# Optimization experiments

Hardware: AMD Instinct MI355X
Metric: run time of the kernel (lower is better)

Reference implementation:

```python
import jax, jax.numpy as jnp
import numpy as np


def setup_inputs() -> dict:
    key = jax.random.key(0)
    k1, k2 = jax.random.split(key)
    B, N, M = 8, 4096, 4096
    points1 = jax.random.normal(k1, (B, N, 3), dtype=jnp.float32)
    points2 = jax.random.normal(k2, (B, M, 3), dtype=jnp.float32)
    return {"points1": points1, "points2": points2}


def reference(points1, points2):
    x2 = jnp.sum(points1 * points1, axis=-1)            # [B, N]
    y2 = jnp.sum(points2 * points2, axis=-1)            # [B, M]
    xy = jnp.einsum('bnd,bmd->bnm', points1, points2)   # [B, N, M]
    d = x2[:, :, None] + y2[:, None, :] - 2.0 * xy      # [B, N, M]
    dist1 = jnp.min(d, axis=2)                          # [B, N] NN dist p1->p2
    dist2 = jnp.min(d, axis=1)                          # [B, M] NN dist p2->p1
    # Symmetric Hausdorff: max over each direction, then max of the two, sum over batch
    m = jnp.maximum(jnp.max(dist1, axis=-1), jnp.max(dist2, axis=-1))  # [B]
    return jnp.sum(m)
```

## Files before the change

### kernel.cpp

```cpp
#include <hip/hip_runtime.h>
#include <float.h>

#define B_CONST 8
#define ONE_BF 0x3F80

typedef short short8 __attribute__((ext_vector_type(8)));
typedef float f32x4  __attribute__((ext_vector_type(4)));

__device__ __forceinline__ unsigned short f2bf(float f) {
    unsigned u = __float_as_uint(f);
    return (unsigned short)((u + 0x7FFFu + ((u >> 16) & 1u)) >> 16);
}
__device__ __forceinline__ float bf2f(unsigned short h) {
    return __uint_as_float(((unsigned)h) << 16);
}
__device__ __forceinline__ float min3(float a, float b, float c) {
    float d;
    asm("v_min3_f32 %0, %1, %2, %3" : "=v"(d) : "v"(a), "v"(b), "v"(c));
    return d;
}

__global__ __launch_bounds__(256) void hd_mfma(
    const float* __restrict__ p1, const float* __restrict__ p2,
    float* __restrict__ part_row, float* __restrict__ part_col,
    unsigned int* __restrict__ comm, int N, int M) {
    int t = threadIdx.x;
    int blk = blockIdx.x;
    if (blk == 0 && t < 9) comm[t] = 0u;

    int gCount  = M >> 10;
    int rbCount = N >> 7;
    int perB = rbCount * gCount;
    int b   = blk / perB;
    int rem = blk - b * perB;
    int rb  = rem / gCount;
    int g   = rem - rb * gCount;

    __shared__ unsigned short ldsBlo[8192];
    __shared__ unsigned short ldsBhi[8192];
    __shared__ unsigned short ldsA0[1024];
    __shared__ unsigned short ldsA1[512];
    __shared__ unsigned int   ldsColU[1024];
    __shared__ float          ldsRow[128];
    __shared__ unsigned short ldsZero[8];

    if (t < 8) ldsZero[t] = 0;
    for (int i = t; i < 1024; i += 256) ldsColU[i] = 0x7F7FFFFFu;

    const float* rsrc = p2 + 3 * ((size_t)b * M + ((size_t)g << 10));
    for (int i = t; i < 1024; i += 256) {
        float x = rsrc[3*i], y = rsrc[3*i+1], z = rsrc[3*i+2];
        unsigned short hx = f2bf(x), hy = f2bf(y), hz = f2bf(z);
        float ex = x - bf2f(hx), ey = y - bf2f(hy), ez = z - bf2f(hz);
        unsigned short m2ex = f2bf(-2.f*ex), m2ey = f2bf(-2.f*ey), m2ez = f2bf(-2.f*ez);
        float rw = fmaf(x,x,fmaf(y,y,z*z));
        unsigned short hrw = f2bf(rw);
        unsigned short erw = f2bf(rw - bf2f(hrw));
        unsigned* lo = (unsigned*)(ldsBlo + i*8);
        lo[0] = hx | ((unsigned)hy << 16);
        lo[1] = hz | ((unsigned)hx << 16);
        lo[2] = hy | ((unsigned)hz << 16);
        lo[3] = m2ex | ((unsigned)m2ey << 16);
        unsigned* hi = (unsigned*)(ldsBhi + i*8);
        hi[0] = m2ez | ((unsigned)hrw << 16);
        hi[1] = erw | ((unsigned)ONE_BF << 16);
        hi[2] = ONE_BF;
        hi[3] = 0;
    }
    const float* qsrc = p1 + 3 * ((size_t)b * N + ((size_t)rb << 7));
    if (t < 128) {
        float x = qsrc[3*t], y = qsrc[3*t+1], z = qsrc[3*t+2];
        unsigned short hx = f2bf(x), hy = f2bf(y), hz = f2bf(z);
        float ex = x - bf2f(hx), ey = y - bf2f(hy), ez = z - bf2f(hz);
        float qw = fmaf(x,x,fmaf(y,y,z*z));
        unsigned short hqw = f2bf(qw);
        unsigned short eqw = f2bf(qw - bf2f(hqw));
        unsigned* a0 = (unsigned*)(ldsA0 + t*8);
        a0[0] = f2bf(-2.f*bf2f(hx)) | ((unsigned)f2bf(-2.f*bf2f(hy)) << 16);
        a0[1] = f2bf(-2.f*bf2f(hz)) | ((unsigned)f2bf(-2.f*ex) << 16);
        a0[2] = f2bf(-2.f*ey) | ((unsigned)f2bf(-2.f*ez) << 16);
        a0[3] = hx | ((unsigned)hy << 16);
        unsigned* a1 = (unsigned*)(ldsA1 + t*4);
        a1[0] = hz | ((unsigned)hqw << 16);
        a1[1] = eqw;
    }
    __syncthreads();

    int l = t & 63, w = t >> 6;
    int n = l & 15, quad = l >> 4;
    const unsigned short* bbase = (quad == 0) ? (ldsBlo + n*8)
                                : (quad == 1) ? (ldsBhi + n*8) : ldsZero;
    int bstride = (quad < 2) ? 128 : 0;

    f32x4 zacc = {0.f, 0.f, 0.f, 0.f};

    for (int s = w; s < 8; s += 4) {
        int qhat = (s << 4) + n;
        short8 af;
        {
            short8 a0v = *(const short8*)(ldsA0 + qhat*8);
            unsigned short hz_ = ldsA1[qhat*4], hqw = ldsA1[qhat*4+1], eqw = ldsA1[qhat*4+2];
            short8 ahi = { (short)hz_, (short)ONE_BF, (short)ONE_BF,
                           (short)hqw, (short)eqw, 0, 0, 0 };
            short8 az = {0,0,0,0,0,0,0,0};
            af = (quad == 0) ? a0v : (quad == 1) ? ahi : az;
        }
        float rm0 = FLT_MAX, rm1 = FLT_MAX, rm2 = FLT_MAX, rm3 = FLT_MAX;
        #pragma unroll 4
        for (int j = 0; j < 64; ++j) {
            short8 bf = *(const short8*)(bbase + j * bstride);
            f32x4 D = __builtin_amdgcn_mfma_f32_16x16x32_bf16(af, bf, zacc, 0, 0, 0);
            rm0 = fminf(rm0, D[0]); rm1 = fminf(rm1, D[1]);
            rm2 = fminf(rm2, D[2]); rm3 = fminf(rm3, D[3]);
            float cm = fminf(min3(D[0], D[1], D[2]), D[3]);
            atomicMin(&ldsColU[(j << 4) + n], __float_as_uint(cm));
        }
        #pragma unroll
        for (int msk = 1; msk < 16; msk <<= 1) {
            rm0 = fminf(rm0, __shfl_xor(rm0, msk, 64));
            rm1 = fminf(rm1, __shfl_xor(rm1, msk, 64));
            rm2 = fminf(rm2, __shfl_xor(rm2, msk, 64));
            rm3 = fminf(rm3, __shfl_xor(rm3, msk, 64));
        }
        if (n == 0) {
            float* rr = ldsRow + (s << 4) + (quad << 2);
            rr[0] = rm0; rr[1] = rm1; rr[2] = rm2; rr[3] = rm3;
        }
    }
    __syncthreads();

    if (t < 128)
        part_row[((size_t)g * B_CONST + b) * N + ((size_t)rb << 7) + t] =
            fmaxf(ldsRow[t], 0.f);
    for (int i = t; i < 1024; i += 256)
        part_col[((size_t)b * rbCount + rb) * M + ((size_t)g << 10) + i] =
            fmaxf(__uint_as_float(ldsColU[i]), 0.f);
}

__global__ __launch_bounds__(256) void hd_final(
    const float* __restrict__ part_row, const float* __restrict__ part_col,
    unsigned int* __restrict__ comm, float* __restrict__ out, int N, int M) {
    int db  = blockIdx.x >> 3;
    int qs  = blockIdx.x & 7;
    int dir = db >> 3;
    int bb  = db & 7;
    int G   = dir ? (N >> 7) : (M >> 10);
    int QN  = dir ? M : N;
    const float* base = dir ? part_col + (size_t)bb * (N >> 7) * M
                            : part_row + (size_t)bb * N;
    size_t gstride = dir ? (size_t)M : (size_t)B_CONST * N;

    int span = QN >> 3;
    int q0 = qs * span;
    float mx = 0.f;
    for (int qq = q0 + threadIdx.x; qq < q0 + span; qq += 256) {
        float mm = base[qq];
        for (int gg = 1; gg < G; ++gg)
            mm = fminf(mm, base[(size_t)gg * gstride + qq]);
        mx = fmaxf(mx, mm);
    }
    #pragma unroll
    for (int off = 32; off > 0; off >>= 1)
        mx = fmaxf(mx, __shfl_down(mx, off, 64));
    __shared__ float wred[4];
    int l = threadIdx.x & 63, w = threadIdx.x >> 6;
    if (l == 0) wred[w] = mx;
    __syncthreads();
    if (threadIdx.x == 0) {
        mx = fmaxf(fmaxf(wred[0], wred[1]), fmaxf(wred[2], wred[3]));
        atomicMax(&comm[bb], __float_as_uint(mx));
        __threadfence();
        unsigned int t2 = atomicAdd(&comm[8], 1u);
        if (t2 == 127u) {
            float s = 0.f;
            for (int k = 0; k < B_CONST; ++k)
                s += __uint_as_float(atomicMax(&comm[k], 0u));
            out[0] = s;
        }
    }
}

extern "C" void kernel_launch(void* const* d_in, const int* in_sizes, int n_in,
                              void* d_out, int out_size, void* d_ws, size_t ws_size,
                              hipStream_t stream) {
    const float* p1 = (const float*)d_in[0];
    const float* p2 = (const float*)d_in[1];
    const int B = B_CONST;
    int N = in_sizes[0] / (3 * B);
    int M = in_sizes[1] / (3 * B);

    float* part_row = (float*)d_ws;
    float* part_col = part_row + (size_t)(M >> 10) * B * N;
    unsigned int* comm = (unsigned int*)(part_col + (size_t)(N >> 7) * B * M);

    int blocks = B * (N >> 7) * (M >> 10);
    hd_mfma<<<blocks, 256, 0, stream>>>(p1, p2, part_row, part_col, comm, N, M);
    hd_final<<<128, 256, 0, stream>>>(part_row, part_col, comm, (float*)d_out, N, M);
}
```

Baseline: 96.66 us.

## Keep all query fragments in registers and split column tiles across waves

The work split inside a block changes: each wave now holds all eight query-row A fragments in registers and owns a disjoint range of 16 column tiles, where before each wave owned query rows and swept every column. Because each wave owns its columns outright, the per-iteration LDS atomicMin on column minima goes away and is replaced by cross-lane shuffles and a plain LDS store. Row minima become per-wave partials, combined after the barrier. The costs are higher register pressure from A[8] and rm[8][4], and one more LDS reduction step for rows.

```diff
diff --git a/kernel.cpp b/kernel.cpp
--- a/kernel.cpp
+++ b/kernel.cpp
@@ -2,7 +2,7 @@
 #include <float.h>
 
 #define B_CONST 8
-#define ONE_BF 0x3F80
+#define ONE_BF 0x3F80u
 
 typedef short short8 __attribute__((ext_vector_type(8)));
 typedef float f32x4  __attribute__((ext_vector_type(4)));
@@ -39,13 +39,12 @@
     __shared__ unsigned short ldsBlo[8192];
     __shared__ unsigned short ldsBhi[8192];
     __shared__ unsigned short ldsA0[1024];
-    __shared__ unsigned short ldsA1[512];
-    __shared__ unsigned int   ldsColU[1024];
-    __shared__ float          ldsRow[128];
+    __shared__ unsigned short ldsAhi[1024];
     __shared__ unsigned short ldsZero[8];
+    __shared__ float ldsCol[1024];
+    __shared__ float ldsRowW[512];
 
     if (t < 8) ldsZero[t] = 0;
-    for (int i = t; i < 1024; i += 256) ldsColU[i] = 0x7F7FFFFFu;
 
     const float* rsrc = p2 + 3 * ((size_t)b * M + ((size_t)g << 10));
     for (int i = t; i < 1024; i += 256) {
@@ -63,7 +62,7 @@
         lo[3] = m2ex | ((unsigned)m2ey << 16);
         unsigned* hi = (unsigned*)(ldsBhi + i*8);
         hi[0] = m2ez | ((unsigned)hrw << 16);
-        hi[1] = erw | ((unsigned)ONE_BF << 16);
+        hi[1] = erw | (ONE_BF << 16);
         hi[2] = ONE_BF;
         hi[3] = 0;
     }
@@ -80,61 +79,77 @@
         a0[1] = f2bf(-2.f*bf2f(hz)) | ((unsigned)f2bf(-2.f*ex) << 16);
         a0[2] = f2bf(-2.f*ey) | ((unsigned)f2bf(-2.f*ez) << 16);
         a0[3] = hx | ((unsigned)hy << 16);
-        unsigned* a1 = (unsigned*)(ldsA1 + t*4);
-        a1[0] = hz | ((unsigned)hqw << 16);
-        a1[1] = eqw;
+        unsigned* ah = (unsigned*)(ldsAhi + t*8);
+        ah[0] = hz | (ONE_BF << 16);
+        ah[1] = ONE_BF | ((unsigned)hqw << 16);
+        ah[2] = eqw;
+        ah[3] = 0;
     }
     __syncthreads();
 
     int l = t & 63, w = t >> 6;
     int n = l & 15, quad = l >> 4;
-    const unsigned short* bbase = (quad == 0) ? (ldsBlo + n*8)
-                                : (quad == 1) ? (ldsBhi + n*8) : ldsZero;
-    int bstride = (quad < 2) ? 128 : 0;
+
+    const unsigned short* abase = (quad == 0) ? ldsA0 : (quad == 1) ? ldsAhi : ldsZero;
+    int astride = (quad < 2) ? 8 : 0;
+    short8 A[8];
+    #pragma unroll
+    for (int s = 0; s < 8; ++s)
+        A[s] = *(const short8*)(abase + ((s << 4) + n) * astride);
+
+    const unsigned short* bbase = (quad == 0) ? ldsBlo : (quad == 1) ? ldsBhi : ldsZero;
+    int bstride = (quad < 2) ? 8 : 0;
 
     f32x4 zacc = {0.f, 0.f, 0.f, 0.f};
-
-    for (int s = w; s < 8; s += 4) {
-        int qhat = (s << 4) + n;
-        short8 af;
-        {
-            short8 a0v = *(const short8*)(ldsA0 + qhat*8);
-            unsigned short hz_ = ldsA1[qhat*4], hqw = ldsA1[qhat*4+1], eqw = ldsA1[qhat*4+2];
-            short8 ahi = { (short)hz_, (short)ONE_BF, (short)ONE_BF,
-                           (short)hqw, (short)eqw, 0, 0, 0 };
-            short8 az = {0,0,0,0,0,0,0,0};
-            af = (quad == 0) ? a0v : (quad == 1) ? ahi : az;
-        }
-        float rm0 = FLT_MAX, rm1 = FLT_MAX, rm2 = FLT_MAX, rm3 = FLT_MAX;
-        #pragma unroll 4
-        for (int j = 0; j < 64; ++j) {
-            short8 bf = *(const short8*)(bbase + j * bstride);
-            f32x4 D = __builtin_amdgcn_mfma_f32_16x16x32_bf16(af, bf, zacc, 0, 0, 0);
-            rm0 = fminf(rm0, D[0]); rm1 = fminf(rm1, D[1]);
-            rm2 = fminf(rm2, D[2]); rm3 = fminf(rm3, D[3]);
-            float cm = fminf(min3(D[0], D[1], D[2]), D[3]);
-            atomicMin(&ldsColU[(j << 4) + n], __float_as_uint(cm));
-        }
+    float rm[8][4];
+    #pragma unroll
+    for (int s = 0; s < 8; ++s)
+        { rm[s][0]=FLT_MAX; rm[s][1]=FLT_MAX; rm[s][2]=FLT_MAX; rm[s][3]=FLT_MAX; }
+
+    for (int j = (w << 4); j < (w << 4) + 16; ++j) {
+        short8 Bf = *(const short8*)(bbase + ((j << 4) + n) * bstride);
+        float cm = FLT_MAX;
+        #pragma unroll
+        for (int s = 0; s < 8; ++s) {
+            f32x4 D = __builtin_amdgcn_mfma_f32_16x16x32_bf16(A[s], Bf, zacc, 0, 0, 0);
+            rm[s][0] = fminf(rm[s][0], D[0]);
+            rm[s][1] = fminf(rm[s][1], D[1]);
+            rm[s][2] = fminf(rm[s][2], D[2]);
+            rm[s][3] = fminf(rm[s][3], D[3]);
+            cm = fminf(cm, fminf(min3(D[0], D[1], D[2]), D[3]));
+        }
+        cm = fminf(cm, __shfl_xor(cm, 16, 64));
+        cm = fminf(cm, __shfl_xor(cm, 32, 64));
+        if (quad == 0) ldsCol[(j << 4) + n] = cm;
+    }
+
+    #pragma unroll
+    for (int s = 0; s < 8; ++s) {
         #pragma unroll
         for (int msk = 1; msk < 16; msk <<= 1) {
-            rm0 = fminf(rm0, __shfl_xor(rm0, msk, 64));
-            rm1 = fminf(rm1, __shfl_xor(rm1, msk, 64));
-            rm2 = fminf(rm2, __shfl_xor(rm2, msk, 64));
-            rm3 = fminf(rm3, __shfl_xor(rm3, msk, 64));
-        }
-        if (n == 0) {
-            float* rr = ldsRow + (s << 4) + (quad << 2);
-            rr[0] = rm0; rr[1] = rm1; rr[2] = rm2; rr[3] = rm3;
+            rm[s][0] = fminf(rm[s][0], __shfl_xor(rm[s][0], msk, 64));
+            rm[s][1] = fminf(rm[s][1], __shfl_xor(rm[s][1], msk, 64));
+            rm[s][2] = fminf(rm[s][2], __shfl_xor(rm[s][2], msk, 64));
+            rm[s][3] = fminf(rm[s][3], __shfl_xor(rm[s][3], msk, 64));
+        }
+    }
+    if (n == 0) {
+        #pragma unroll
+        for (int s = 0; s < 8; ++s) {
+            float* rr = ldsRowW + (w << 7) + (s << 4) + (quad << 2);
+            rr[0] = rm[s][0]; rr[1] = rm[s][1]; rr[2] = rm[s][2]; rr[3] = rm[s][3];
         }
     }
     __syncthreads();
 
-    if (t < 128)
-        part_row[((size_t)g * B_CONST + b) * N + ((size_t)rb << 7) + t] =
-            fmaxf(ldsRow[t], 0.f);
+    if (t < 128) {
+        float m = fminf(fminf(ldsRowW[t], ldsRowW[128 + t]),
+                        fminf(ldsRowW[256 + t], ldsRowW[384 + t]));
+        part_row[((size_t)g * B_CONST + b) * N + ((size_t)rb << 7) + t] = fmaxf(m, 0.f);
+    }
     for (int i = t; i < 1024; i += 256)
         part_col[((size_t)b * rbCount + rb) * M + ((size_t)g << 10) + i] =
-            fmaxf(__uint_as_float(ldsColU[i]), 0.f);
+            fmaxf(ldsCol[i], 0.f);
 }
 
 __global__ __launch_bounds__(256) void hd_final(
```

New measurement: 108.2 us. +11.9%, slower.
